# Kernel tuning notes

Hardware: AMD Instinct MI355X
Metric: run time of the kernel (lower is better)

The kernel has to match this reference:

```python
import jax, jax.numpy as jnp
import numpy as np

P = 12           # AR order == number of rollout steps
N = 2048         # input_size (nodes)
B = 128          # batch
C = 1            # channels (only channel 0 used)


def setup_inputs() -> dict:
    key = jax.random.key(0)
    kx, kw = jax.random.split(key)
    x = jax.random.normal(kx, (B, N, C, P), dtype=jnp.float32)
    W = jax.random.normal(kw, (P, N, N), dtype=jnp.float32)
    return {"x": x, "W": W}


def reference(x, W):
    # x: [B, N, C, L]; take channel 0 and transpose -> [B, L(=p), N]
    xt = jnp.transpose(x[:, :, 0, :], (0, 2, 1))

    def step(xc, _):
        # einsum('ijk,bik->bij') followed by sum over i fuses to 'ijk,bik->bj'
        y = jnp.einsum('ijk,bik->bj', W, xc)              # [B, N]
        xc = jnp.concatenate([xc[:, 1:, :], y[:, None, :]], axis=1)  # shift window
        return xc, y

    _, ys = jax.lax.scan(step, xt, None, length=12)       # ys: [12, B, N]
    return jnp.transpose(ys, (1, 2, 0))                   # [B, N, 12]
```

## Files before the change

### kernel.cpp

```cpp
#include <hip/hip_runtime.h>
#include <stdint.h>


typedef _Float16 f16x8 __attribute__((ext_vector_type(8)));
typedef float    f32x4 __attribute__((ext_vector_type(4)));

#define B_ 128
#define N_ 2048
#define P_ 12
#define K_ (P_*N_)
#define KSPLIT 32
#define KCH (K_/KSPLIT)
#define NPHASE (KCH/64)
#define NTILES 16
#define NKP (K_/64)

#define WPK_BYTES   ((size_t)NTILES*NKP*16384)
#define H_SLOT_BYTES ((size_t)B_*N_*2)
#define H_BYTES     (23*H_SLOT_BYTES)
#define PART_BYTES  ((size_t)KSPLIT*B_*N_*2)
#define WS_NEEDED   (WPK_BYTES + H_BYTES + PART_BYTES)

__device__ __constant__ int E_TAB[11] = {7, 13, 18, 24, 29, 35, 40, 46, 51, 57, 62};

__device__ __forceinline__ int e_of_slot(int g) {
    return (g < 12) ? 0 : E_TAB[g - 12];
}
__device__ __forceinline__ float pow2f(int e) {
    return __uint_as_float((uint32_t)(127 + e) << 23);
}

union F16x8 { _Float16 h[8]; uint4 q; };
union F16x4v { _Float16 h[4]; uint2 q; };

__device__ __forceinline__ uint32_t h_off(int slot, int b, int k) {
    return (uint32_t)slot * (uint32_t)H_SLOT_BYTES
         + (uint32_t)(k >> 5) * 8192u + (uint32_t)(((k >> 3) & 3) << 11)
         + (uint32_t)(b << 4) + (uint32_t)((k & 7) << 1);
}

__device__ __forceinline__ size_t w_tile_base(int nt, int pk) {
    return ((size_t)nt * NKP + (size_t)pk) * 16384;
}

__global__ void prep_w(const float* __restrict__ W, char* __restrict__ Wp) {
    __shared__ float tile[128][68];
    int id = blockIdx.x;
    int nt = id / NKP, pk = id % NKP;
    int i = pk >> 5;
    int k0 = (pk & 31) << 6;
    int j0 = nt << 7;
    int t = threadIdx.x;
    #pragma unroll
    for (int pass = 0; pass < 8; ++pass) {
        int jl = pass * 16 + (t >> 4);
        int kq = (t & 15) * 4;
        float4 v = *(const float4*)(W + ((size_t)i * N_ + (j0 + jl)) * N_ + k0 + kq);
        tile[jl][kq + 0] = v.x; tile[jl][kq + 1] = v.y;
        tile[jl][kq + 2] = v.z; tile[jl][kq + 3] = v.w;
    }
    __syncthreads();
    int ksub = t >> 7, c = t & 127;
    char* base = Wp + w_tile_base(nt, pk) + (ksub << 13);
    #pragma unroll
    for (int ko = 0; ko < 4; ++ko) {
        F16x8 o;
        #pragma unroll
        for (int q = 0; q < 8; ++q) o.h[q] = (_Float16)tile[c][ksub * 32 + ko * 8 + q];
        uint32_t off = (uint32_t)((c << 6) + (ko << 4)) ^ (uint32_t)((c & 7) << 4);
        *(uint4*)(base + off) = o.q;
    }
}

__global__ void prep_x(const float* __restrict__ x, char* __restrict__ H) {
    int tid = blockIdx.x * 256 + threadIdx.x;
    int b = tid >> 8;
    int n0 = (tid & 255) << 3;
    const float4* s4 = (const float4*)(x + ((size_t)b * N_ + n0) * P_);
    float4 tmp[24];
    #pragma unroll
    for (int i2 = 0; i2 < 24; ++i2) tmp[i2] = s4[i2];
    #pragma unroll
    for (int p = 0; p < 12; ++p) {
        F16x8 o;
        #pragma unroll
        for (int q = 0; q < 8; ++q) {
            int fi = q * 12 + p;
            float4 blk = tmp[fi >> 2];
            float f = ((fi & 3) == 0) ? blk.x : ((fi & 3) == 1) ? blk.y : ((fi & 3) == 2) ? blk.z : blk.w;
            o.h[q] = (_Float16)f;
        }
        *(uint4*)(H + h_off(p, b, n0)) = o.q;
    }
}

__global__ __launch_bounds__(256, 2) void gemm_step(
        const char* __restrict__ Wp, const char* __restrict__ H,
        _Float16* __restrict__ partial, int st)
{
    __shared__ alignas(16) char ldsB[2][16384];
    const int tid  = threadIdx.x;
    const int lane = tid & 63;
    const int wv   = tid >> 6;
    const int wr   = wv >> 1;
    const int wc   = wv & 1;
    const int bid  = blockIdx.x;
    const int ks    = bid % KSPLIT;
    const int ntile = bid / KSPLIT;
    const int jbase = (ntile << 7) + (wc << 6) + (lane & 15);
    const int ko   = lane >> 4;
    const int kbase = ks * KCH;
    const int pk0  = kbase >> 6;

    uint32_t boff[4];
    #pragma unroll
    for (int nf = 0; nf < 4; ++nf) {
        int c = (wc << 6) + (nf << 4) + (lane & 15);
        boff[nf] = (uint32_t)((c << 6) + (ko << 4)) ^ (uint32_t)((c & 7) << 4);
    }

    auto stage = [&](int buf, int ph) {
        const char* src = Wp + w_tile_base(ntile, pk0 + ph);
        #pragma unroll
        for (int j = 0; j < 4; ++j) {
            uint32_t o = (uint32_t)(j << 12) + (uint32_t)(tid << 4);
            __builtin_amdgcn_global_load_lds(
                (const __attribute__((address_space(1))) void*)(src + o),
                (__attribute__((address_space(3))) void*)&ldsB[buf][(j << 12) + (wv << 10)], 16, 0, 0);
        }
    };
    auto loadA = [&](int ph, f16x8 a[2][4]) {
        #pragma unroll
        for (int ksub = 0; ksub < 2; ++ksub) {
            int kg = kbase + (ph << 6) + (ksub << 5);
            const char* sb = H + (size_t)(st + (kg >> 11)) * H_SLOT_BYTES
                           + (uint32_t)(((kg & 2047) >> 5) << 13) + (uint32_t)(ko << 11);
            #pragma unroll
            for (int m = 0; m < 4; ++m) {
                int brow = (wr << 6) + (m << 4) + (lane & 15);
                a[ksub][m] = *(const f16x8*)(sb + (brow << 4));
            }
        }
    };

    f32x4 acc[4][4];
    #pragma unroll
    for (int m = 0; m < 4; ++m)
        #pragma unroll
        for (int n = 0; n < 4; ++n) acc[m][n] = (f32x4){0.f, 0.f, 0.f, 0.f};

    f16x8 a[2][4];
    loadA(0, a);
    stage(0, 0);
    __syncthreads();

    int cur_e = e_of_slot(st + (kbase >> 11));
    for (int ph = 0; ph < NPHASE; ++ph) {
        int e_new = e_of_slot(st + ((kbase + (ph << 6)) >> 11));
        if (e_new != cur_e) {
            float f = pow2f(cur_e - e_new);
            #pragma unroll
            for (int m = 0; m < 4; ++m)
                #pragma unroll
                for (int n = 0; n < 4; ++n) acc[m][n] *= f;
            cur_e = e_new;
        }
        if (ph + 1 < NPHASE) stage((ph & 1) ^ 1, ph + 1);
        const char* lb = &ldsB[ph & 1][0];
        f16x8 bf[2][4];
        #pragma unroll
        for (int ksub = 0; ksub < 2; ++ksub)
            #pragma unroll
            for (int nf = 0; nf < 4; ++nf)
                bf[ksub][nf] = *(const f16x8*)(lb + (ksub << 13) + boff[nf]);
        f16x8 an[2][4];
        if (ph + 1 < NPHASE) loadA(ph + 1, an);
        #pragma unroll
        for (int ksub = 0; ksub < 2; ++ksub)
            #pragma unroll
            for (int m = 0; m < 4; ++m)
                #pragma unroll
                for (int nf = 0; nf < 4; ++nf)
                    acc[m][nf] = __builtin_amdgcn_mfma_f32_16x16x32_f16(a[ksub][m], bf[ksub][nf], acc[m][nf], 0, 0, 0);
        #pragma unroll
        for (int ksub = 0; ksub < 2; ++ksub)
            #pragma unroll
            for (int m = 0; m < 4; ++m) a[ksub][m] = an[ksub][m];
        __syncthreads();
    }

    const int r0 = (lane >> 4) << 2;
    _Float16* pb = partial + ((size_t)ks * B_ + (wr << 6) + r0) * N_ + jbase;
    #pragma unroll
    for (int m = 0; m < 4; ++m)
        #pragma unroll
        for (int n = 0; n < 4; ++n)
            #pragma unroll
            for (int r = 0; r < 4; ++r)
                pb[(size_t)(m * 16 + r) * N_ + n * 16] = (_Float16)acc[m][n][r];
}

__global__ void reduce_step(const _Float16* __restrict__ partial, float* __restrict__ out,
                            char* __restrict__ H, int t)
{
    int tid = blockIdx.x * 256 + threadIdx.x;
    int b = tid >> 9;
    int n0 = (tid & 511) << 2;
    float s0 = 0.f, s1 = 0.f, s2 = 0.f, s3 = 0.f;
    #pragma unroll 4
    for (int c = 0; c < KSPLIT; ++c) {
        float sc = pow2f(e_of_slot(t + ((c * KCH + (KCH - 64)) >> 11)));
        F16x4v p;
        p.q = *(const uint2*)(partial + ((size_t)c * B_ + b) * N_ + n0);
        s0 += (float)p.h[0] * sc; s1 += (float)p.h[1] * sc;
        s2 += (float)p.h[2] * sc; s3 += (float)p.h[3] * sc;
    }
    float* ob = out + ((size_t)b * N_ + n0) * P_ + t;
    ob[0 * P_] = s0; ob[1 * P_] = s1; ob[2 * P_] = s2; ob[3 * P_] = s3;
    if (t < 11) {
        float ds = pow2f(-E_TAB[t]);
        F16x4v o;
        o.h[0] = (_Float16)(s0 * ds); o.h[1] = (_Float16)(s1 * ds);
        o.h[2] = (_Float16)(s2 * ds); o.h[3] = (_Float16)(s3 * ds);
        *(uint2*)(H + h_off(12 + t, b, n0)) = o.q;
    }
}

__global__ void naive_step(const float* __restrict__ x, const float* __restrict__ W,
                           float* __restrict__ out, int t)
{
    int tid = blockIdx.x * 256 + threadIdx.x;
    int b = tid >> 11;
    int j = tid & (N_ - 1);
    float acc = 0.f;
    for (int i = 0; i < 12; ++i) {
        int g = t + i;
        const float* src = (g < 12) ? (x   + (size_t)b * (N_ * 12) + g)
                                    : (out + (size_t)b * (N_ * 12) + (g - 12));
        const float* wr = W + ((size_t)i * N_ + j) * N_;
        for (int k = 0; k < N_; ++k)
            acc += wr[k] * src[(size_t)k * 12];
    }
    out[((size_t)b * N_ + j) * 12 + t] = acc;
}

extern "C" void kernel_launch(void* const* d_in, const int* in_sizes, int n_in,
                              void* d_out, int out_size, void* d_ws, size_t ws_size,
                              hipStream_t stream)
{
    const float* x = (const float*)d_in[0];
    const float* W = (const float*)d_in[1];
    float* out = (float*)d_out;

    if (ws_size < WS_NEEDED) {
        for (int t = 0; t < 12; ++t)
            naive_step<<<1024, 256, 0, stream>>>(x, W, out, t);
        return;
    }

    char* ws = (char*)d_ws;
    char* Wp = ws;
    char* H  = Wp + WPK_BYTES;
    _Float16* partial = (_Float16*)(H + H_BYTES);

    prep_w<<<6144, 256, 0, stream>>>(W, Wp);
    prep_x<<<128, 256, 0, stream>>>(x, H);
    for (int t = 0; t < 12; ++t) {
        gemm_step<<<512, 256, 0, stream>>>(Wp, H, partial, t);
        reduce_step<<<256, 256, 0, stream>>>(partial, out, H, t);
    }
}
```

Baseline: 451.7 us.

## Double K-step per pipeline phase and merge weight/input prep kernels

The GEMM step now processes 128 K-elements per phase instead of 64, staging two packed W tiles (32 KB per buffer) per barrier. This halves the number of __syncthreads and loop iterations and gives more MFMA work per stage to hide global-to-LDS latency. It costs double the LDS (64 KB per block) and more A-fragment registers, which may reduce occupancy. The separate W-pack and x-pack prep kernels are also fused into one launch, saving a kernel launch.

```diff
diff --git a/kernel.cpp b/kernel.cpp
--- a/kernel.cpp
+++ b/kernel.cpp
@@ -11,7 +11,7 @@
 #define K_ (P_*N_)
 #define KSPLIT 32
 #define KCH (K_/KSPLIT)
-#define NPHASE (KCH/64)
+#define NPHASE (KCH/128)
 #define NTILES 16
 #define NKP (K_/64)
 
@@ -43,14 +43,38 @@
     return ((size_t)nt * NKP + (size_t)pk) * 16384;
 }
 
-__global__ void prep_w(const float* __restrict__ W, char* __restrict__ Wp) {
+__global__ void prep_all(const float* __restrict__ x, const float* __restrict__ W,
+                         char* __restrict__ Wp, char* __restrict__ H)
+{
     __shared__ float tile[128][68];
-    int id = blockIdx.x;
-    int nt = id / NKP, pk = id % NKP;
-    int i = pk >> 5;
+    int bid = blockIdx.x, t = threadIdx.x;
+    if (bid < 128) {
+        int tg = bid * 256 + t;
+        int b = tg >> 8;
+        int n0 = (tg & 255) << 3;
+        const float4* s4 = (const float4*)(x + ((size_t)b * N_ + n0) * P_);
+        float4 tmp[24];
+        #pragma unroll
+        for (int i2 = 0; i2 < 24; ++i2) tmp[i2] = s4[i2];
+        #pragma unroll
+        for (int p = 0; p < 12; ++p) {
+            F16x8 o;
+            #pragma unroll
+            for (int q = 0; q < 8; ++q) {
+                int fi = q * 12 + p;
+                float4 blk = tmp[fi >> 2];
+                float f = ((fi & 3) == 0) ? blk.x : ((fi & 3) == 1) ? blk.y : ((fi & 3) == 2) ? blk.z : blk.w;
+                o.h[q] = (_Float16)f;
+            }
+            *(uint4*)(H + h_off(p, b, n0)) = o.q;
+        }
+        return;
+    }
+    int u = bid - 128;
+    int nt = u / NKP, pk = u % NKP;
+    int i  = pk >> 5;
     int k0 = (pk & 31) << 6;
     int j0 = nt << 7;
-    int t = threadIdx.x;
     #pragma unroll
     for (int pass = 0; pass < 8; ++pass) {
         int jl = pass * 16 + (t >> 4);
@@ -72,33 +96,11 @@
     }
 }
 
-__global__ void prep_x(const float* __restrict__ x, char* __restrict__ H) {
-    int tid = blockIdx.x * 256 + threadIdx.x;
-    int b = tid >> 8;
-    int n0 = (tid & 255) << 3;
-    const float4* s4 = (const float4*)(x + ((size_t)b * N_ + n0) * P_);
-    float4 tmp[24];
-    #pragma unroll
-    for (int i2 = 0; i2 < 24; ++i2) tmp[i2] = s4[i2];
-    #pragma unroll
-    for (int p = 0; p < 12; ++p) {
-        F16x8 o;
-        #pragma unroll
-        for (int q = 0; q < 8; ++q) {
-            int fi = q * 12 + p;
-            float4 blk = tmp[fi >> 2];
-            float f = ((fi & 3) == 0) ? blk.x : ((fi & 3) == 1) ? blk.y : ((fi & 3) == 2) ? blk.z : blk.w;
-            o.h[q] = (_Float16)f;
-        }
-        *(uint4*)(H + h_off(p, b, n0)) = o.q;
-    }
-}
-
 __global__ __launch_bounds__(256, 2) void gemm_step(
         const char* __restrict__ Wp, const char* __restrict__ H,
         _Float16* __restrict__ partial, int st)
 {
-    __shared__ alignas(16) char ldsB[2][16384];
+    __shared__ alignas(16) char ldsB[2][32768];
     const int tid  = threadIdx.x;
     const int lane = tid & 63;
     const int wv   = tid >> 6;
@@ -120,19 +122,19 @@
     }
 
     auto stage = [&](int buf, int ph) {
-        const char* src = Wp + w_tile_base(ntile, pk0 + ph);
-        #pragma unroll
-        for (int j = 0; j < 4; ++j) {
+        const char* src = Wp + w_tile_base(ntile, pk0 + (ph << 1));
+        #pragma unroll
+        for (int j = 0; j < 8; ++j) {
             uint32_t o = (uint32_t)(j << 12) + (uint32_t)(tid << 4);
             __builtin_amdgcn_global_load_lds(
                 (const __attribute__((address_space(1))) void*)(src + o),
                 (__attribute__((address_space(3))) void*)&ldsB[buf][(j << 12) + (wv << 10)], 16, 0, 0);
         }
     };
-    auto loadA = [&](int ph, f16x8 a[2][4]) {
-        #pragma unroll
-        for (int ksub = 0; ksub < 2; ++ksub) {
-            int kg = kbase + (ph << 6) + (ksub << 5);
+    auto loadA = [&](int ph, f16x8 a[4][4]) {
+        #pragma unroll
+        for (int ksub = 0; ksub < 4; ++ksub) {
+            int kg = kbase + (ph << 7) + (ksub << 5);
             const char* sb = H + (size_t)(st + (kg >> 11)) * H_SLOT_BYTES
                            + (uint32_t)(((kg & 2047) >> 5) << 13) + (uint32_t)(ko << 11);
             #pragma unroll
@@ -149,14 +151,15 @@
         #pragma unroll
         for (int n = 0; n < 4; ++n) acc[m][n] = (f32x4){0.f, 0.f, 0.f, 0.f};
 
-    f16x8 a[2][4];
+    f16x8 a[4][4];
     loadA(0, a);
     stage(0, 0);
     __syncthreads();
 
     int cur_e = e_of_slot(st + (kbase >> 11));
+    #pragma unroll 1
     for (int ph = 0; ph < NPHASE; ++ph) {
-        int e_new = e_of_slot(st + ((kbase + (ph << 6)) >> 11));
+        int e_new = e_of_slot(st + ((kbase + (ph << 7)) >> 11));
         if (e_new != cur_e) {
             float f = pow2f(cur_e - e_new);
             #pragma unroll
@@ -166,24 +169,23 @@
             cur_e = e_new;
         }
         if (ph + 1 < NPHASE) stage((ph & 1) ^ 1, ph + 1);
+        f16x8 an[4][4];
+        if (ph + 1 < NPHASE) loadA(ph + 1, an);
         const char* lb = &ldsB[ph & 1][0];
-        f16x8 bf[2][4];
-        #pragma unroll
-        for (int ksub = 0; ksub < 2; ++ksub)
+        #pragma unroll
+        for (int ksub = 0; ksub < 4; ++ksub) {
+            f16x8 bf[4];
             #pragma unroll
             for (int nf = 0; nf < 4; ++nf)
-                bf[ksub][nf] = *(const f16x8*)(lb + (ksub << 13) + boff[nf]);
-        f16x8 an[2][4];
-        if (ph + 1 < NPHASE) loadA(ph + 1, an);
-        #pragma unroll
-        for (int ksub = 0; ksub < 2; ++ksub)
+                bf[nf] = *(const f16x8*)(lb + (ksub << 13) + boff[nf]);
             #pragma unroll
             for (int m = 0; m < 4; ++m)
                 #pragma unroll
                 for (int nf = 0; nf < 4; ++nf)
-                    acc[m][nf] = __builtin_amdgcn_mfma_f32_16x16x32_f16(a[ksub][m], bf[ksub][nf], acc[m][nf], 0, 0, 0);
-        #pragma unroll
-        for (int ksub = 0; ksub < 2; ++ksub)
+                    acc[m][nf] = __builtin_amdgcn_mfma_f32_16x16x32_f16(a[ksub][m], bf[nf], acc[m][nf], 0, 0, 0);
+        }
+        #pragma unroll
+        for (int ksub = 0; ksub < 4; ++ksub)
             #pragma unroll
             for (int m = 0; m < 4; ++m) a[ksub][m] = an[ksub][m];
         __syncthreads();
@@ -263,8 +265,7 @@
     char* H  = Wp + WPK_BYTES;
     _Float16* partial = (_Float16*)(H + H_BYTES);
 
-    prep_w<<<6144, 256, 0, stream>>>(W, Wp);
-    prep_x<<<128, 256, 0, stream>>>(x, H);
+    prep_all<<<6272, 256, 0, stream>>>(x, W, Wp, H);
     for (int t = 0; t < 12; ++t) {
         gemm_step<<<512, 256, 0, stream>>>(Wp, H, partial, t);
         reduce_step<<<256, 256, 0, stream>>>(partial, out, H, t);
```

After: 539.8 us. 1.2x slower.
